# Kernel optimization log

Hardware: AMD Instinct MI355X
Metric: run time of the kernel (lower is better)

The kernel has to match this reference:

```python
import jax, jax.numpy as jnp
import numpy as np
from jax import lax

N, CIN, COUT, T, V, G, K = 32, 64, 64, 256, 25, 8, 3  # batch, channels, time, joints, groups, subsets
EPS = 1e-5  # BatchNorm eps


def setup_inputs() -> dict:
    key = jax.random.key(0)
    ks = jax.random.split(key, 10)
    x = jax.random.normal(ks[0], (N, CIN, T, V), jnp.float32)
    # DecoupleA param: A reshaped [3,1,V,V] tiled over groups (torch .repeat tiles)
    A0 = jax.random.uniform(ks[1], (K, 1, V, V), jnp.float32)
    DecoupleA = jnp.tile(A0, (1, G, 1, 1))
    W = jax.random.normal(ks[2], (CIN, COUT * K), jnp.float32) * np.float32(np.sqrt(0.5 / (COUT * K)))
    b = jnp.full((1, COUT * K, 1, 1), 1e-6, jnp.float32)
    g0 = 1.0 + 0.1 * jax.random.normal(ks[3], (COUT * K,), jnp.float32)
    b0 = 0.1 * jax.random.normal(ks[4], (COUT * K,), jnp.float32)
    g1 = 1.0 + 0.1 * jax.random.normal(ks[5], (COUT,), jnp.float32)
    b1 = 0.1 * jax.random.normal(ks[6], (COUT,), jnp.float32)
    conv_w = jax.random.normal(ks[7], (COUT, COUT, 9, 1), jnp.float32) * np.float32(np.sqrt(2.0 / (COUT * 9)))
    conv_b = jnp.zeros((COUT,), jnp.float32)
    g2 = 1.0 + 0.1 * jax.random.normal(ks[8], (COUT,), jnp.float32)
    b2 = 0.1 * jax.random.normal(ks[9], (COUT,), jnp.float32)
    return {"x": x, "DecoupleA": DecoupleA, "W": W, "b": b, "g0": g0, "b0": b0,
            "g1": g1, "b1": b1, "conv_w": conv_w, "conv_b": conv_b, "g2": g2, "b2": b2,
            "keep_prob": 1}


def _bn_eval(y, g, be):
    # inference BN with running_mean=0, running_var=1
    return y * (g / jnp.sqrt(1.0 + EPS))[None, :, None, None] + be[None, :, None, None]


def reference(x, DecoupleA, W, b, g0, b0, g1, b1, conv_w, conv_b, g2, b2, keep_prob):
    # ---- unit_gcn ----
    learn_A = jnp.tile(DecoupleA, (1, COUT // G, 1, 1))           # [3, COUT, V, V]
    # norm(): right-multiply by diag((colsum + 0.001)^-1) == scale columns
    invD = 1.0 / (jnp.sum(learn_A, axis=2) + 0.001)               # [3, COUT, V]
    normA = learn_A * invD[:, :, None, :]
    y = jnp.einsum('nctw,cd->ndtw', x, W) + b                     # [N, 3*COUT, T, V]
    y = _bn_eval(y, g0, b0)
    y = y.reshape(N, K, COUT, T, V)
    y = jnp.einsum('nkctv,kcvw->nctw', y, normA)                  # message passing
    y = _bn_eval(y, g1, b1)
    y = jax.nn.relu(y + x)                                        # down = identity (CIN==COUT)
    # ---- unit_tcn (keep_prob==1 -> DropBlocks are identity) ----
    z = lax.conv_general_dilated(y, conv_w, (1, 1), [(4, 4), (0, 0)],
                                 dimension_numbers=('NCHW', 'OIHW', 'NCHW'))
    z = z + conv_b[None, :, None, None]
    z = _bn_eval(z, g2, b2)
    # ---- residual (identity, CIN==COUT, stride=1; skip-DropBlocks identity) ----
    return jax.nn.relu(z + x)
```

## Files before the change

kernel.cpp:

```cpp
#include <hip/hip_runtime.h>
#include <hip/hip_bf16.h>
#include <stdint.h>


typedef const float* fp;
typedef __attribute__((ext_vector_type(8))) short short8;
typedef __attribute__((ext_vector_type(4))) float floatx4;

__device__ __forceinline__ float us2f(unsigned int u){
  union { unsigned int i; float f; } c; c.i = u << 16; return c.f;
}
__device__ __forceinline__ unsigned short f2us(float f){
  __hip_bfloat16 h = __float2bfloat16(f);
  return *reinterpret_cast<unsigned short*>(&h);
}
__device__ __forceinline__ void gload_lds16(const void* g, void* l){
  __builtin_amdgcn_global_load_lds(
      (const __attribute__((address_space(1))) void*)g,
      (__attribute__((address_space(3))) void*)l, 16, 0, 0);
}


__global__ __launch_bounds__(256) void k_prep(
    fp x, fp A, fp W, fp b, fp g0, fp b0, fp g1, fp b1,
    fp cw, fp cb, fp g2, fp b2,
    unsigned short* U, float* biasU, unsigned short* xb,
    float* cbe, unsigned short* cwetb)
{
  int bid = blockIdx.x, tid = threadIdx.x;
  const float inv_s = rsqrtf(1.0f + 1e-5f);
  __shared__ __align__(16) char smemraw[26624];

  if (bid < 1024) {
    int n = bid >> 5, tb = bid & 31, t0 = tb*8;
    unsigned short* xs = (unsigned short*)smemraw;
    for (int e4 = tid; e4 < 3200; e4 += 256) {
      int c = e4 / 50, r4 = (e4 - c*50)*4;
      floatx4 xv = *(const floatx4*)(x + (long long)(n*64 + c)*6400 + t0*25 + r4);
      int tt = r4 / 25, v = r4 - tt*25;
      xs[(c*8 + tt)*26 + v] = f2us(xv.x); if (++v == 25){v = 0; tt++;}
      xs[(c*8 + tt)*26 + v] = f2us(xv.y); if (++v == 25){v = 0; tt++;}
      xs[(c*8 + tt)*26 + v] = f2us(xv.z); if (++v == 25){v = 0; tt++;}
      xs[(c*8 + tt)*26 + v] = f2us(xv.w);
    }
    __syncthreads();
    for (int e4 = tid; e4 < 3200; e4 += 256) {
      int base = e4 * 4;
      int tt = base / 1600, q0 = base - tt*1600;
      int c = q0 / 25, v = q0 - c*25;
      ushort4 pk;
      pk.x = xs[(c*8 + tt)*26 + v]; if (++v == 25){v = 0; c++;}
      pk.y = xs[(c*8 + tt)*26 + v]; if (++v == 25){v = 0; c++;}
      pk.z = xs[(c*8 + tt)*26 + v]; if (++v == 25){v = 0; c++;}
      pk.w = xs[(c*8 + tt)*26 + v];
      *(ushort4*)(xb + (long long)(n*256 + t0 + tt)*1600 + q0) = pk;
    }
    return;
  }

  if (bid < 2816) {
    int m = bid - 1024;
    if (m >= 1600) {
      if (tid < 200) {
        short8 z = (short8){0,0,0,0,0,0,0,0};
        *(short8*)(U + (long long)m*1600 + tid*8) = z;
      }
      return;
    }
    float* nAL   = (float*)smemraw;
    float* WeffL = (float*)(smemraw + 512);
    float* cs3   = (float*)(smemraw + 1408);
    int c = m & 63, w = m >> 6, g = c & 7;
    if (tid < 75) {
      int kk = tid / 25, vv = tid % 25;
      nAL[tid] = A[((kk*8 + g)*25 + vv)*25 + w];
    }
    if (tid < 192) {
      int kk = tid >> 6, cin = tid & 63;
      WeffL[tid] = W[cin*192 + kk*64 + c] * (g0[kk*64 + c] * inv_s);
    }
    __syncthreads();
    if (tid < 3) {
      float s = 0.f;
      for (int vv = 0; vv < 25; vv++) s += nAL[tid*25 + vv];
      cs3[tid] = s + 0.001f;
    }
    __syncthreads();
    if (tid < 75) nAL[tid] = nAL[tid] / cs3[tid/25];
    __syncthreads();
    float s1 = g1[c] * inv_s;
    if (tid < 200) {
      int k0 = tid * 8;
      short8 pk;
      #pragma unroll
      for (int q = 0; q < 8; q++) {
        int k = k0 + q;
        int cin = k / 25, vv = k - cin*25;
        float acc = WeffL[cin]       * nAL[vv]
                  + WeffL[64 + cin]  * nAL[25 + vv]
                  + WeffL[128 + cin] * nAL[50 + vv];
        acc *= s1;
        if (cin == c && vv == w) acc += 1.0f;
        pk[q] = (short)f2us(acc);
      }
      *(short8*)(U + (long long)m*1600 + k0) = pk;
    }
    if (tid == 0) {
      float acc = 0.f;
      for (int kk = 0; kk < 3; kk++) {
        int d = kk*64 + c;
        float be = b[d] * (g0[d] * inv_s) + b0[d];
        for (int v = 0; v < 25; v++) acc += be * nAL[kk*25 + v];
      }
      biasU[m] = acc * s1 + b1[c];
    }
    return;
  }

  int gid = (bid - 2816)*256 + tid;
  if (gid < 36864) {
    int o = gid / 576, r = gid % 576;
    int j = r / 64, i = r % 64;
    cwetb[gid] = f2us(cw[(o*64+i)*9 + j] * (g2[o] * inv_s));
    return;
  }
  gid -= 36864;
  if (gid < 64) {
    cbe[gid] = cb[gid] * (g2[gid] * inv_s) + b2[gid];
  }
}

__global__ __launch_bounds__(512, 4) void k_gemm(
    const unsigned short* U, const unsigned short* xb, const float* biasU,
    unsigned short* yb)
{
  int bm = blockIdx.x >> 6, bn = blockIdx.x & 63;
  int n = bn >> 1, t0 = (bn & 1) * 128;
  int tid = threadIdx.x, lane = tid & 63, wid = tid >> 6;
  int l15 = lane & 15, grp = lane >> 4;

  __shared__ __align__(16) unsigned short As[256*64];
  __shared__ __align__(16) unsigned short Bs[128*64];

  const unsigned short* gA[4];
  const unsigned short* gB[2];
  unsigned short* lA[4];
  unsigned short* lB[2];
  #pragma unroll
  for (int it = 0; it < 4; it++) {
    int e = it*512 + tid;
    int row = e >> 3, li = e & 7;
    int kcol = (li ^ (row & 7)) * 8;
    gA[it] = U + (long long)(bm*256 + row)*1600 + kcol;
    lA[it] = As + e*8;
  }
  #pragma unroll
  for (int it = 0; it < 2; it++) {
    int e = it*512 + tid;
    int row = e >> 3, li = e & 7;
    int kcol = (li ^ (row & 7)) * 8;
    gB[it] = xb + (long long)(n*256 + t0 + row)*1600 + kcol;
    lB[it] = Bs + e*8;
  }

  floatx4 acc[2][8];
  #pragma unroll
  for (int i = 0; i < 2; i++)
    #pragma unroll
    for (int j = 0; j < 8; j++) acc[i][j] = (floatx4){0.f,0.f,0.f,0.f};

  for (int kc = 0; kc < 25; kc++) {
    #pragma unroll
    for (int it = 0; it < 4; it++) gload_lds16(gA[it] + kc*64, lA[it]);
    #pragma unroll
    for (int it = 0; it < 2; it++) gload_lds16(gB[it] + kc*64, lB[it]);
    __syncthreads();
    #pragma unroll
    for (int ks = 0; ks < 2; ks++) {
      int colk = ((ks*4 + grp) ^ (l15 & 7)) * 8;
      short8 af[2], bf[8];
      #pragma unroll
      for (int i = 0; i < 2; i++)
        af[i] = *(const short8*)(As + (wid*32 + i*16 + l15)*64 + colk);
      #pragma unroll
      for (int j = 0; j < 8; j++)
        bf[j] = *(const short8*)(Bs + (j*16 + l15)*64 + colk);
      #pragma unroll
      for (int i = 0; i < 2; i++)
        #pragma unroll
        for (int j = 0; j < 8; j++)
          acc[i][j] = __builtin_amdgcn_mfma_f32_16x16x32_bf16(af[i], bf[j], acc[i][j], 0, 0, 0);
    }
    __syncthreads();
  }

  #pragma unroll
  for (int i = 0; i < 2; i++) {
    int mbase = bm*256 + wid*32 + i*16 + grp*4;
    if (mbase >= 1600) continue;
    float4 bu = *(const float4*)(biasU + mbase);
    #pragma unroll
    for (int j = 0; j < 8; j++) {
      int col = j*16 + l15;
      int t = t0 + col;
      ushort4 pk;
      pk.x = f2us(fmaxf(acc[i][j][0] + bu.x, 0.f));
      pk.y = f2us(fmaxf(acc[i][j][1] + bu.y, 0.f));
      pk.z = f2us(fmaxf(acc[i][j][2] + bu.z, 0.f));
      pk.w = f2us(fmaxf(acc[i][j][3] + bu.w, 0.f));
      *(ushort4*)(yb + (long long)(n*256 + t)*1600 + mbase) = pk;
    }
  }
}

__global__ __launch_bounds__(512) void k_tcn(
    const unsigned short* yb, const unsigned short* cwetb, const float* cbe,
    fp x, const unsigned short* zpg, float* out)
{
  int n = blockIdx.x >> 4, tb = blockIdx.x & 15, t0 = tb*16;
  int tid = threadIdx.x, lane = tid & 63, wid = tid >> 6;
  int l15 = lane & 15, grp = lane >> 4;
  __shared__ __align__(16) unsigned short ys[5120*8];

  #pragma unroll
  for (int it = 0; it < 6; it++) {
    int e = it*512 + tid;
    int row = e >> 3, li = e & 7;
    int rt = row / 25, v = row - rt*25;
    int tg = t0 - 4 + rt;
    int sli = li ^ (row & 7);
    bool ok = (tg >= 0) && (tg < 256);
    const unsigned short* src = ok
      ? yb + ((long long)(n*256 + tg)*1600 + v*64 + sli*8)
      : zpg + li*8;
    gload_lds16(src, ys + e*8);
  }

  int p = wid & 3, h = wid >> 2;
  int o0 = p * 16;
  int o = o0 + l15;
  short8 af[9][2];
  #pragma unroll
  for (int j = 0; j < 9; j++) {
    af[j][0] = *(const short8*)(cwetb + ((o*9 + j)*64 + grp*8));
    af[j][1] = *(const short8*)(cwetb + ((o*9 + j)*64 + 32 + grp*8));
  }
  float4 cb4 = *(const float4*)(cbe + o0 + grp*4);
  __syncthreads();

  #pragma unroll
  for (int it = 6; it < 10; it++) {
    int e = it*512 + tid;
    int row = e >> 3, li = e & 7;
    int rt = row / 25, v = row - rt*25;
    int tg = t0 - 4 + rt;
    int sli = li ^ (row & 7);
    bool ok = (row < 600) && (tg >= 0) && (tg < 256);
    const unsigned short* src = ok
      ? yb + ((long long)(n*256 + tg)*1600 + v*64 + sli*8)
      : zpg + li*8;
    gload_lds16(src, ys + e*8);
  }

  #pragma unroll 1
  for (int phase = 0; phase < 2; phase++) {
    int tstart = phase ? (12 - h) : h;
    int tend   = phase ? 25 : 11;
    for (int tile = tstart; tile < tend; tile += 2) {
      int colb = tile*16 + l15;
      floatx4 accA = (floatx4){0.f,0.f,0.f,0.f};
      floatx4 accB = (floatx4){0.f,0.f,0.f,0.f};
      #pragma unroll
      for (int j = 0; j < 9; j++) {
        int row = colb + 25*j;
        int r7 = row & 7;
        const unsigned short* rb = ys + row*64;
        short8 b0 = *(const short8*)(rb + ((grp     ^ r7))*8);
        short8 b1 = *(const short8*)(rb + (((4+grp) ^ r7))*8);
        if (j & 1) {
          accB = __builtin_amdgcn_mfma_f32_16x16x32_bf16(af[j][0], b0, accB, 0, 0, 0);
          accB = __builtin_amdgcn_mfma_f32_16x16x32_bf16(af[j][1], b1, accB, 0, 0, 0);
        } else {
          accA = __builtin_amdgcn_mfma_f32_16x16x32_bf16(af[j][0], b0, accA, 0, 0, 0);
          accA = __builtin_amdgcn_mfma_f32_16x16x32_bf16(af[j][1], b1, accA, 0, 0, 0);
        }
      }
      if (colb < 400) {
        int tt = colb / 25, v = colb - tt*25, t = t0 + tt;
        #pragma unroll
        for (int r = 0; r < 4; r++) {
          int oo = o0 + grp*4 + r;
          float val = accA[r] + accB[r] + ((const float*)&cb4)[r]
                    + x[((n*64 + oo)*256 + t)*25 + v];
          out[((n*64 + oo)*256 + t)*25 + v] = fmaxf(val, 0.f);
        }
      }
    }
    if (phase == 0) __syncthreads();
  }
}

extern "C" void kernel_launch(void* const* d_in, const int* in_sizes, int n_in,
                              void* d_out, int out_size, void* d_ws, size_t ws_size,
                              hipStream_t stream)
{
  fp x  = (fp)d_in[0];
  fp A  = (fp)d_in[1];
  fp W  = (fp)d_in[2];
  fp b  = (fp)d_in[3];
  fp g0 = (fp)d_in[4];
  fp b0 = (fp)d_in[5];
  fp g1 = (fp)d_in[6];
  fp b1 = (fp)d_in[7];
  fp cw = (fp)d_in[8];
  fp cb = (fp)d_in[9];
  fp g2 = (fp)d_in[10];
  fp b2 = (fp)d_in[11];

  char* ws = (char*)d_ws;
  float*          cbe   = (float*)(ws + 117504);
  unsigned short* cwetb = (unsigned short*)(ws + 117760);
  float*          biasU = (float*)(ws + 191488);
  unsigned short* U     = (unsigned short*)(ws + 197888);
  unsigned short* xb    = (unsigned short*)(ws + 5932288);
  unsigned short* yb    = (unsigned short*)(ws + 32146688);
  const unsigned short* zpg = U + (long long)1600*1600;

  k_prep<<<2961, 256, 0, stream>>>(x, A, W, b, g0, b0, g1, b1, cw, cb, g2, b2,
                                   U, biasU, xb, cbe, cwetb);
  k_gemm<<<448, 512, 0, stream>>>(U, xb, biasU, yb);
  k_tcn<<<512, 512, 0, stream>>>(yb, cwetb, cbe, x, zpg, (float*)d_out);
}
```

Measured before the change: 206.6 us.

## Double-buffer LDS tiles in GEMM to overlap global loads with MFMA

Converts the GEMM main loop from a single 64-wide K tile per iteration to double-buffered 32-wide K tiles, prefetching the next tile with direct global-to-LDS loads while MFMAs consume the current one. The XOR swizzle is adjusted to the 4-chunk rows. This is meant to hide global load latency behind compute. In exchange it doubles the iteration count and barriers, and each step does less MFMA work per synchronisation. LDS use per block drops slightly.

```diff
diff --git a/kernel.cpp b/kernel.cpp
--- a/kernel.cpp
+++ b/kernel.cpp
@@ -139,28 +139,19 @@
   int tid = threadIdx.x, lane = tid & 63, wid = tid >> 6;
   int l15 = lane & 15, grp = lane >> 4;
 
-  __shared__ __align__(16) unsigned short As[256*64];
-  __shared__ __align__(16) unsigned short Bs[128*64];
-
-  const unsigned short* gA[4];
-  const unsigned short* gB[2];
-  unsigned short* lA[4];
-  unsigned short* lB[2];
-  #pragma unroll
-  for (int it = 0; it < 4; it++) {
-    int e = it*512 + tid;
-    int row = e >> 3, li = e & 7;
-    int kcol = (li ^ (row & 7)) * 8;
-    gA[it] = U + (long long)(bm*256 + row)*1600 + kcol;
-    lA[it] = As + e*8;
-  }
-  #pragma unroll
-  for (int it = 0; it < 2; it++) {
-    int e = it*512 + tid;
-    int row = e >> 3, li = e & 7;
-    int kcol = (li ^ (row & 7)) * 8;
-    gB[it] = xb + (long long)(n*256 + t0 + row)*1600 + kcol;
-    lB[it] = Bs + e*8;
+  __shared__ __align__(16) unsigned short As[2][256*32];
+  __shared__ __align__(16) unsigned short Bs[2][128*32];
+
+  const unsigned short* gA[2];
+  const unsigned short* gB;
+  int eA0 = tid, eA1 = 512 + tid;
+  {
+    int r0 = eA0 >> 2, l0 = eA0 & 3;
+    int r1 = eA1 >> 2, l1 = eA1 & 3;
+    gA[0] = U + (long long)(bm*256 + r0)*1600 + (l0 ^ (r0 & 3))*8;
+    gA[1] = U + (long long)(bm*256 + r1)*1600 + (l1 ^ (r1 & 3))*8;
+    int rb = tid >> 2, lb = tid & 3;
+    gB = xb + (long long)(n*256 + t0 + rb)*1600 + (lb ^ (rb & 3))*8;
   }
 
   floatx4 acc[2][8];
@@ -169,28 +160,34 @@
     #pragma unroll
     for (int j = 0; j < 8; j++) acc[i][j] = (floatx4){0.f,0.f,0.f,0.f};
 
-  for (int kc = 0; kc < 25; kc++) {
-    #pragma unroll
-    for (int it = 0; it < 4; it++) gload_lds16(gA[it] + kc*64, lA[it]);
-    #pragma unroll
-    for (int it = 0; it < 2; it++) gload_lds16(gB[it] + kc*64, lB[it]);
-    __syncthreads();
-    #pragma unroll
-    for (int ks = 0; ks < 2; ks++) {
-      int colk = ((ks*4 + grp) ^ (l15 & 7)) * 8;
-      short8 af[2], bf[8];
-      #pragma unroll
-      for (int i = 0; i < 2; i++)
-        af[i] = *(const short8*)(As + (wid*32 + i*16 + l15)*64 + colk);
+  int colk = (grp ^ (l15 & 3)) * 8;
+
+  gload_lds16(gA[0], &As[0][eA0*8]);
+  gload_lds16(gA[1], &As[0][eA1*8]);
+  gload_lds16(gB,    &Bs[0][tid*8]);
+  asm volatile("s_waitcnt vmcnt(0)" ::: "memory");
+  __syncthreads();
+
+  for (int kc = 0; kc < 50; kc++) {
+    int cur = kc & 1, nxt = cur ^ 1;
+    if (kc < 49) {
+      gload_lds16(gA[0] + (kc+1)*32, &As[nxt][eA0*8]);
+      gload_lds16(gA[1] + (kc+1)*32, &As[nxt][eA1*8]);
+      gload_lds16(gB    + (kc+1)*32, &Bs[nxt][tid*8]);
+    }
+    short8 af[2], bf[8];
+    #pragma unroll
+    for (int i = 0; i < 2; i++)
+      af[i] = *(const short8*)(&As[cur][(wid*32 + i*16 + l15)*32 + colk]);
+    #pragma unroll
+    for (int j = 0; j < 8; j++)
+      bf[j] = *(const short8*)(&Bs[cur][(j*16 + l15)*32 + colk]);
+    #pragma unroll
+    for (int i = 0; i < 2; i++)
       #pragma unroll
       for (int j = 0; j < 8; j++)
-        bf[j] = *(const short8*)(Bs + (j*16 + l15)*64 + colk);
-      #pragma unroll
-      for (int i = 0; i < 2; i++)
-        #pragma unroll
-        for (int j = 0; j < 8; j++)
-          acc[i][j] = __builtin_amdgcn_mfma_f32_16x16x32_bf16(af[i], bf[j], acc[i][j], 0, 0, 0);
-    }
+        acc[i][j] = __builtin_amdgcn_mfma_f32_16x16x32_bf16(af[i], bf[j], acc[i][j], 0, 0, 0);
+    asm volatile("s_waitcnt vmcnt(0)" ::: "memory");
     __syncthreads();
   }
 
```

Result: slower. 216.7 us (+4.9%).
